# Optimization experiments

Measured on AMD Instinct MI355X. Metric: run time of the kernel, lower is better.

## Reference

```python
import jax, jax.numpy as jnp
import numpy as np

EPS = 1e-6
NUM_HEADS = 16

def _ln(x):
    # LayerNorm32, no affine, eps=1e-6, computed in fp32
    x32 = x.astype(jnp.float32)
    mu = jnp.mean(x32, axis=-1, keepdims=True)
    var = jnp.var(x32, axis=-1, keepdims=True)
    return ((x32 - mu) * jax.lax.rsqrt(var + EPS)).astype(x.dtype)

def _mha(q, k, v):
    # q,k,v: [B, L, H, D]
    d = q.shape[-1]
    scale = 1.0 / jnp.sqrt(jnp.asarray(d, q.dtype))
    s = jnp.einsum('bqhd,bkhd->bhqk', q, k) * scale
    p = jax.nn.softmax(s, axis=-1)
    o = jnp.einsum('bhqk,bkhd->bqhd', p, v)
    return o.reshape(o.shape[0], o.shape[1], -1)

def setup_inputs() -> dict:
    key = jax.random.key(0)
    ks = jax.random.split(key, 10)
    B, L, C, Lc, Cc = 4, 2048, 1024, 1024, 1024
    Dff = 4 * C
    s = 0.02
    return {
        'x': jax.random.normal(ks[0], (B, L, C), jnp.float32),
        'context': jax.random.normal(ks[1], (B, Lc, Cc), jnp.float32),
        'w_qkv': jax.random.normal(ks[2], (C, 3 * C), jnp.float32) * s,
        'b_qkv': jnp.zeros((3 * C,), jnp.float32),
        'w_os': jax.random.normal(ks[3], (C, C), jnp.float32) * s,
        'b_os': jnp.zeros((C,), jnp.float32),
        'w_qc': jax.random.normal(ks[4], (C, C), jnp.float32) * s,
        'b_qc': jnp.zeros((C,), jnp.float32),
        'w_kvc': jax.random.normal(ks[5], (Cc, 2 * C), jnp.float32) * s,
        'b_kvc': jnp.zeros((2 * C,), jnp.float32),
        'w_oc': jax.random.normal(ks[6], (C, C), jnp.float32) * s,
        'b_oc': jnp.zeros((C,), jnp.float32),
        'w_fc1': jax.random.normal(ks[7], (C, Dff), jnp.float32) * s,
        'b_fc1': jnp.zeros((Dff,), jnp.float32),
        'w_fc2': jax.random.normal(ks[8], (Dff, C), jnp.float32) * s,
        'b_fc2': jnp.zeros((C,), jnp.float32),
    }

def reference(x, context, w_qkv, b_qkv, w_os, b_os, w_qc, b_qc, w_kvc, b_kvc,
              w_oc, b_oc, w_fc1, b_fc1, w_fc2, b_fc2):
    B, L, C = x.shape
    H = NUM_HEADS
    D = C // H
    # --- self attention (pre-norm, full) ---
    h = _ln(x)
    qkv = (h @ w_qkv + b_qkv).reshape(B, L, 3, H, D)
    q, k, v = qkv[:, :, 0], qkv[:, :, 1], qkv[:, :, 2]
    h = _mha(q, k, v) @ w_os + b_os
    x = x + h
    # --- cross attention ---
    h = _ln(x)
    q = (h @ w_qc + b_qc).reshape(B, L, H, D)
    Lc = context.shape[1]
    kv = (context @ w_kvc + b_kvc).reshape(B, Lc, 2, H, D)
    k, v = kv[:, :, 0], kv[:, :, 1]
    h = _mha(q, k, v) @ w_oc + b_oc
    x = x + h
    # --- sparse FFN (GELU tanh) ---
    h = _ln(x)
    h = jax.nn.gelu(h @ w_fc1 + b_fc1, approximate=True) @ w_fc2 + b_fc2
    return x + h
```

## Files before the change

kernel.cpp:

```cpp
#include <hip/hip_runtime.h>

typedef unsigned short ushort_t;
typedef __attribute__((ext_vector_type(8))) short short8;
typedef __attribute__((ext_vector_type(4))) float f32x4;
typedef __attribute__((ext_vector_type(4))) unsigned short ushort4v;

__device__ inline ushort_t f2bf(float f) {
    union { float f; unsigned u; } v; v.f = f;
    return (ushort_t)((v.u + 0x7FFFu + ((v.u >> 16) & 1u)) >> 16);
}
__device__ inline float bf2f(ushort_t u) {
    union { unsigned u; float f; } v; v.u = ((unsigned)u) << 16;
    return v.f;
}

__device__ inline float fast_exp2(float x) {
#if __has_builtin(__builtin_amdgcn_exp2f)
    return __builtin_amdgcn_exp2f(x);
#else
    float r; asm("v_exp_f32 %0, %1" : "=v"(r) : "v"(x)); return r;
#endif
}

__device__ inline void gld16(const ushort_t* g, ushort_t* l) {
    __builtin_amdgcn_global_load_lds(
        (const __attribute__((address_space(1))) unsigned int*)g,
        (__attribute__((address_space(3))) unsigned int*)l, 16, 0, 0);
}

__device__ inline int xcd_swz(int id, int nwg) {
    int q = nwg >> 3;
    return (id & 7) * q + (id >> 3);
}

struct WPrep {
    const float* src[7];
    ushort_t*    dst[7];
    int K[7], N[7];
    int tilesBefore[8];
};

__global__ void w_prep_all(WPrep P) {
    __shared__ float t[64][65];
    const int bid = blockIdx.x;
    int e = 0;
#pragma unroll
    for (int i = 0; i < 7; i++) if (bid >= P.tilesBefore[i + 1]) e = i + 1;
    const int lt = bid - P.tilesBefore[e];
    const int K = P.K[e], N = P.N[e];
    const int ntx = N >> 6;
    const int n0 = (lt % ntx) * 64, k0 = (lt / ntx) * 64;
    const float* w = P.src[e];
    ushort_t* out = P.dst[e];
    const int tid = threadIdx.x;
#pragma unroll
    for (int i = 0; i < 16; i++) {
        int idx = tid + i * 256;
        int r = idx >> 6, c = idx & 63;
        t[r][c] = w[(size_t)(k0 + r) * N + n0 + c];
    }
    __syncthreads();
#pragma unroll
    for (int i = 0; i < 16; i++) {
        int idx = tid + i * 256;
        int nr = idx >> 6, kc = idx & 63;
        out[(size_t)(n0 + nr) * K + k0 + kc] = f2bf(t[kc][nr]);
    }
}

__global__ void v_transpose(const ushort_t* __restrict__ V, int vStride, int rowsPerBatch,
                            ushort_t* __restrict__ Vt, int Lk) {
    __shared__ __align__(16) ushort_t t[64][72];
    const int bh = blockIdx.y, k0 = blockIdx.x * 64;
    const int b = bh >> 4, h = bh & 15;
    const int tid = threadIdx.x;
    const ushort_t* src = V + (size_t)(b * rowsPerBatch + k0) * vStride + h * 64;
#pragma unroll
    for (int i = 0; i < 2; i++) {
        int ch = tid + i * 256;
        int r = ch >> 3, c = (ch & 7) * 8;
        *(short8*)(&t[r][c]) = *(const short8*)(src + (size_t)r * vStride + c);
    }
    __syncthreads();
#pragma unroll
    for (int i = 0; i < 2; i++) {
        int ch = tid + i * 256;
        int d = ch >> 3, c = (ch & 7) * 8;
        short8 o;
#pragma unroll
        for (int j = 0; j < 8; j++) o[j] = (short)t[c + j][d];
        *(short8*)(Vt + ((size_t)bh * 64 + d) * Lk + k0 + c) = o;
    }
}

__global__ void f32_to_bf16_vec(const float* __restrict__ in, ushort_t* __restrict__ out, int n4) {
    int i = blockIdx.x * blockDim.x + threadIdx.x;
    if (i < n4) {
        float4 v = ((const float4*)in)[i];
        ushort4v o;
        o[0] = f2bf(v.x); o[1] = f2bf(v.y); o[2] = f2bf(v.z); o[3] = f2bf(v.w);
        ((ushort4v*)out)[i] = o;
    }
}

__global__ void ln_rows(const float* __restrict__ in, ushort_t* __restrict__ out) {
    __shared__ float s1[4], s2[4];
    const int row = blockIdx.x;
    const int tid = threadIdx.x;
    const float4 v = ((const float4*)(in + (size_t)row * 1024))[tid];
    float s  = v.x + v.y + v.z + v.w;
    float ss = v.x * v.x + v.y * v.y + v.z * v.z + v.w * v.w;
#pragma unroll
    for (int d = 32; d >= 1; d >>= 1) {
        s  += __shfl_down(s, d, 64);
        ss += __shfl_down(ss, d, 64);
    }
    if ((tid & 63) == 0) { s1[tid >> 6] = s; s2[tid >> 6] = ss; }
    __syncthreads();
    float sum = s1[0] + s1[1] + s1[2] + s1[3];
    float sqs = s2[0] + s2[1] + s2[2] + s2[3];
    float mu  = sum * (1.0f / 1024.0f);
    float var = sqs * (1.0f / 1024.0f) - mu * mu;
    float rs  = rsqrtf(var + 1e-6f);
    ushort4v o;
    o[0] = f2bf((v.x - mu) * rs);
    o[1] = f2bf((v.y - mu) * rs);
    o[2] = f2bf((v.z - mu) * rs);
    o[3] = f2bf((v.w - mu) * rs);
    ((ushort4v*)(out + (size_t)row * 1024))[tid] = o;
}

#define EPI_BF16 0
#define EPI_GELU 1
#define EPI_RES  2

template <int EPI>
__global__ void gemm_bt(const ushort_t* __restrict__ A, const ushort_t* __restrict__ Bt,
                        const float* __restrict__ bias, const float* __restrict__ res,
                        void* __restrict__ outp, int M, int N, int K) {
    __shared__ __align__(16) ushort_t As[128 * 64];
    __shared__ __align__(16) ushort_t Bs[128 * 64];
    const int tid = threadIdx.x;
    const int lane = tid & 63, wave = tid >> 6;
    const int nwg = gridDim.x * gridDim.y;
    const int sid = xcd_swz(blockIdx.y * gridDim.x + blockIdx.x, nwg);
    const int m0 = (sid / gridDim.x) * 128, n0 = (sid % gridDim.x) * 128;
    const int wr = (wave >> 1) * 64, wc = (wave & 1) * 64;
    const int lr = lane & 15, lg = lane >> 4;

    f32x4 acc[4][4];
#pragma unroll
    for (int i = 0; i < 4; i++)
#pragma unroll
        for (int j = 0; j < 4; j++) acc[i][j] = f32x4{0.f, 0.f, 0.f, 0.f};

    for (int k0 = 0; k0 < K; k0 += 64) {
#pragma unroll
        for (int i = 0; i < 4; i++) {
            int ch = tid + i * 256;
            int r = ch >> 3;
            int kcs = (((ch & 7) ^ (r & 7))) * 8;
            gld16(A  + (size_t)(m0 + r) * K + k0 + kcs, As + ch * 8);
            gld16(Bt + (size_t)(n0 + r) * K + k0 + kcs, Bs + ch * 8);
        }
        __syncthreads();
#pragma unroll
        for (int ks = 0; ks < 2; ks++) {
            short8 af[4], bfr[4];
#pragma unroll
            for (int m = 0; m < 4; m++) {
                int r = wr + m * 16 + lr;
                int kc = ks * 4 + lg;
                af[m] = *(const short8*)(As + r * 64 + ((kc ^ (r & 7)) << 3));
            }
#pragma unroll
            for (int n = 0; n < 4; n++) {
                int r = wc + n * 16 + lr;
                int kc = ks * 4 + lg;
                bfr[n] = *(const short8*)(Bs + r * 64 + ((kc ^ (r & 7)) << 3));
            }
#pragma unroll
            for (int m = 0; m < 4; m++)
#pragma unroll
                for (int n = 0; n < 4; n++)
                    acc[m][n] = __builtin_amdgcn_mfma_f32_16x16x32_bf16(af[m], bfr[n], acc[m][n], 0, 0, 0);
        }
        __syncthreads();
    }

#pragma unroll
    for (int m = 0; m < 4; m++) {
        int rowb = m0 + wr + m * 16 + lg * 4;
#pragma unroll
        for (int n = 0; n < 4; n++) {
            int col = n0 + wc + n * 16 + lr;
            float bcol = bias[col];
            f32x4 v = acc[m][n];
#pragma unroll
            for (int q = 0; q < 4; q++) {
                float x = v[q] + bcol;
                if (EPI == EPI_GELU) {
                    float u = 0.7978845608028654f * (x + 0.044715f * x * x * x);
                    float a = fabsf(u);
                    float tt = fast_exp2(-2.885390081777927f * a);
                    float th = copysignf((1.0f - tt) / (1.0f + tt), u);
                    x = 0.5f * x * (1.0f + th);
                }
                size_t off = (size_t)(rowb + q) * N + col;
                if (EPI == EPI_RES) ((float*)outp)[off] = x + res[off];
                else                ((ushort_t*)outp)[off] = f2bf(x);
            }
        }
    }
}

__global__ __launch_bounds__(512, 2)
void attn_fwd(const ushort_t* __restrict__ Q, int qStride,
              const ushort_t* __restrict__ Kp, int kvStride, int kvBatchRows,
              const ushort_t* __restrict__ Vt, int Lk,
              ushort_t* __restrict__ O) {
    __shared__ __align__(16) ushort_t Ks[2][64 * 64];
    __shared__ __align__(16) ushort_t Vts[2][64 * 64];
    __shared__ __align__(16) ushort_t Ps[8][16 * 64];
    const int tid = threadIdx.x, lane = tid & 63, wave = tid >> 6;
    const int lr = lane & 15, lg = lane >> 4;
    const int sid = xcd_swz(blockIdx.x, gridDim.x);
    const int qb = sid & 7, h = (sid >> 3) & 15, b = sid >> 7;
    const int qRow0 = b * 2048 + qb * 256;
    const int kvRow0 = b * kvBatchRows;
    const int hc = h * 64;
    const ushort_t* vt_base = Vt + (size_t)(b * 16 + h) * 64 * Lk;

    short8 qf[2][2];
#pragma unroll
    for (int qh = 0; qh < 2; qh++) {
        const ushort_t* qrow = Q + (size_t)(qRow0 + wave * 32 + qh * 16 + lr) * qStride + hc;
        short8 r0 = *(const short8*)(qrow + lg * 8);
        short8 r1 = *(const short8*)(qrow + 32 + lg * 8);
        const float s = 0.125f * 1.4426950408889634f;
#pragma unroll
        for (int j = 0; j < 8; j++) {
            qf[qh][0][j] = (short)f2bf(bf2f((ushort_t)r0[j]) * s);
            qf[qh][1][j] = (short)f2bf(bf2f((ushort_t)r1[j]) * s);
        }
    }

    f32x4 oacc[2][4];
#pragma unroll
    for (int qh = 0; qh < 2; qh++)
#pragma unroll
        for (int d = 0; d < 4; d++) oacc[qh][d] = f32x4{0.f, 0.f, 0.f, 0.f};
    float mrun[2] = {-1e30f, -1e30f}, lrun[2] = {0.f, 0.f};

    const int nt = Lk >> 6;

    auto stage = [&](int buf, int kt) {
        int r = tid >> 3;
        int kcs = (((tid & 7) ^ (r & 7))) * 8;
        gld16(Kp + (size_t)(kvRow0 + kt + r) * kvStride + hc + kcs, Ks[buf] + tid * 8);
        gld16(vt_base + (size_t)r * Lk + kt + kcs, Vts[buf] + tid * 8);
    };

    stage(0, 0);
    __syncthreads();
    int cur = 0;

    for (int t = 0; t < nt; ++t) {
        if (t + 1 < nt) stage(cur ^ 1, (t + 1) * 64);

        const ushort_t* Kc = Ks[cur];
        const ushort_t* Vc = Vts[cur];

        f32x4 sacc[2][4];
        __builtin_amdgcn_s_setprio(1);
#pragma unroll
        for (int n = 0; n < 4; n++) {
            int r = n * 16 + lr;
            short8 k0 = *(const short8*)(Kc + r * 64 + ((lg ^ (r & 7)) << 3));
            short8 k1 = *(const short8*)(Kc + r * 64 + (((4 + lg) ^ (r & 7)) << 3));
#pragma unroll
            for (int qh = 0; qh < 2; qh++) {
                f32x4 s = f32x4{0.f, 0.f, 0.f, 0.f};
                s = __builtin_amdgcn_mfma_f32_16x16x32_bf16(k0, qf[qh][0], s, 0, 0, 0);
                s = __builtin_amdgcn_mfma_f32_16x16x32_bf16(k1, qf[qh][1], s, 0, 0, 0);
                sacc[qh][n] = s;
            }
        }
        __builtin_amdgcn_s_setprio(0);

        short8 pf[2][2];
        ushort_t* Pw = &Ps[wave][0];
#pragma unroll
        for (int qh = 0; qh < 2; qh++) {
            float mx = sacc[qh][0][0];
#pragma unroll
            for (int n = 0; n < 4; n++)
#pragma unroll
                for (int r = 0; r < 4; r++) if (n | r) mx = fmaxf(mx, sacc[qh][n][r]);
            mx = fmaxf(mx, __shfl_xor(mx, 16, 64));
            mx = fmaxf(mx, __shfl_xor(mx, 32, 64));

            if (!__all(mx <= mrun[qh] + 11.5416f)) {
                float mnew = fmaxf(mrun[qh], mx);
                float al = fast_exp2(mrun[qh] - mnew);
                float a0 = __shfl(al, lg * 4 + 0, 64);
                float a1 = __shfl(al, lg * 4 + 1, 64);
                float a2 = __shfl(al, lg * 4 + 2, 64);
                float a3 = __shfl(al, lg * 4 + 3, 64);
#pragma unroll
                for (int dn = 0; dn < 4; dn++) {
                    oacc[qh][dn][0] *= a0; oacc[qh][dn][1] *= a1;
                    oacc[qh][dn][2] *= a2; oacc[qh][dn][3] *= a3;
                }
                lrun[qh] *= al;
                mrun[qh] = mnew;
            }

            float rsum = 0.f;
#pragma unroll
            for (int n = 0; n < 4; n++)
#pragma unroll
                for (int r = 0; r < 4; r++) {
                    float p = fast_exp2(sacc[qh][n][r] - mrun[qh]);
                    sacc[qh][n][r] = p;
                    rsum += p;
                }
            rsum += __shfl_xor(rsum, 16, 64);
            rsum += __shfl_xor(rsum, 32, 64);
            lrun[qh] += rsum;

#pragma unroll
            for (int n = 0; n < 4; n++) {
                unsigned w0, w1;
                asm("v_cvt_pk_bf16_f32 %0, %1, %2" : "=v"(w0) : "v"(sacc[qh][n][0]), "v"(sacc[qh][n][1]));
                asm("v_cvt_pk_bf16_f32 %0, %1, %2" : "=v"(w1) : "v"(sacc[qh][n][2]), "v"(sacc[qh][n][3]));
                int kc = n * 2 + (lg >> 1);
                uint2 u; u.x = w0; u.y = w1;
                *(uint2*)((char*)Pw + lr * 128 + ((kc ^ (lr & 7)) << 4) + (lg & 1) * 8) = u;
            }
            pf[qh][0] = *(const short8*)(Pw + lr * 64 + ((lg ^ (lr & 7)) << 3));
            pf[qh][1] = *(const short8*)(Pw + lr * 64 + (((4 + lg) ^ (lr & 7)) << 3));
        }

        __builtin_amdgcn_s_setprio(1);
#pragma unroll
        for (int dn = 0; dn < 4; dn++) {
            int r = dn * 16 + lr;
            short8 v0 = *(const short8*)(Vc + r * 64 + ((lg ^ (r & 7)) << 3));
            short8 v1 = *(const short8*)(Vc + r * 64 + (((4 + lg) ^ (r & 7)) << 3));
#pragma unroll
            for (int qh = 0; qh < 2; qh++) {
                oacc[qh][dn] = __builtin_amdgcn_mfma_f32_16x16x32_bf16(pf[qh][0], v0, oacc[qh][dn], 0, 0, 0);
                oacc[qh][dn] = __builtin_amdgcn_mfma_f32_16x16x32_bf16(pf[qh][1], v1, oacc[qh][dn], 0, 0, 0);
            }
        }
        __builtin_amdgcn_s_setprio(0);
        __syncthreads();
        cur ^= 1;
    }

#pragma unroll
    for (int qh = 0; qh < 2; qh++) {
        float linv[4];
#pragma unroll
        for (int r = 0; r < 4; r++) linv[r] = 1.0f / __shfl(lrun[qh], lg * 4 + r, 64);
#pragma unroll
        for (int dn = 0; dn < 4; dn++)
#pragma unroll
            for (int q = 0; q < 4; q++) {
                float o = oacc[qh][dn][q] * linv[q];
                int row = qRow0 + wave * 32 + qh * 16 + lg * 4 + q;
                int col = hc + dn * 16 + lr;
                O[(size_t)row * 1024 + col] = f2bf(o);
            }
    }
}

extern "C" void kernel_launch(void* const* d_in, const int* in_sizes, int n_in,
                              void* d_out, int out_size, void* d_ws, size_t ws_size,
                              hipStream_t stream) {
    const float* x     = (const float*)d_in[0];
    const float* ctx   = (const float*)d_in[1];
    const float* w_qkv = (const float*)d_in[2];
    const float* b_qkv = (const float*)d_in[3];
    const float* w_os  = (const float*)d_in[4];
    const float* b_os  = (const float*)d_in[5];
    const float* w_qc  = (const float*)d_in[6];
    const float* b_qc  = (const float*)d_in[7];
    const float* w_kvc = (const float*)d_in[8];
    const float* b_kvc = (const float*)d_in[9];
    const float* w_oc  = (const float*)d_in[10];
    const float* b_oc  = (const float*)d_in[11];
    const float* w_fc1 = (const float*)d_in[12];
    const float* b_fc1 = (const float*)d_in[13];
    const float* w_fc2 = (const float*)d_in[14];
    const float* b_fc2 = (const float*)d_in[15];
    float* out = (float*)d_out;

    char* ws = (char*)d_ws;
    ushort_t* wqkvT = (ushort_t*)(ws + 0);
    ushort_t* wosT  = (ushort_t*)(ws + 6291456);
    ushort_t* wqcT  = (ushort_t*)(ws + 8388608);
    ushort_t* wkvcT = (ushort_t*)(ws + 10485760);
    ushort_t* wocT  = (ushort_t*)(ws + 14680064);
    ushort_t* wfc1T = (ushort_t*)(ws + 16777216);
    ushort_t* wfc2T = (ushort_t*)(ws + 25165824);
    ushort_t* qkv_bf  = (ushort_t*)(ws + 33554432);
    ushort_t* q_bf    = (ushort_t*)(ws + 33554432);
    ushort_t* kv_bf   = (ushort_t*)(ws + 50331648);
    ushort_t* vt_c    = (ushort_t*)(ws + 67108864);
    ushort_t* ffn_bf  = (ushort_t*)(ws + 33554432);
    ushort_t* ctx_bf  = (ushort_t*)(ws + 83886080);
    ushort_t* attn_bf = (ushort_t*)(ws + 92274688);
    ushort_t* h_bf    = (ushort_t*)(ws + 109051904);
    ushort_t* vt_s    = (ushort_t*)(ws + 109051904);

    const dim3 tb(256);
    const dim3 tb512(512);

    WPrep P;
    P.src[0] = w_qkv; P.dst[0] = wqkvT; P.K[0] = 1024; P.N[0] = 3072;
    P.src[1] = w_os;  P.dst[1] = wosT;  P.K[1] = 1024; P.N[1] = 1024;
    P.src[2] = w_qc;  P.dst[2] = wqcT;  P.K[2] = 1024; P.N[2] = 1024;
    P.src[3] = w_kvc; P.dst[3] = wkvcT; P.K[3] = 1024; P.N[3] = 2048;
    P.src[4] = w_oc;  P.dst[4] = wocT;  P.K[4] = 1024; P.N[4] = 1024;
    P.src[5] = w_fc1; P.dst[5] = wfc1T; P.K[5] = 1024; P.N[5] = 4096;
    P.src[6] = w_fc2; P.dst[6] = wfc2T; P.K[6] = 4096; P.N[6] = 1024;
    P.tilesBefore[0] = 0;
    for (int i = 0; i < 7; i++)
        P.tilesBefore[i + 1] = P.tilesBefore[i] + (P.N[i] / 64) * (P.K[i] / 64);
    w_prep_all<<<dim3(P.tilesBefore[7]), tb, 0, stream>>>(P);
    f32_to_bf16_vec<<<4096, tb, 0, stream>>>(ctx, ctx_bf, 1048576);

    ln_rows<<<8192, tb, 0, stream>>>(x, h_bf);
    gemm_bt<EPI_BF16><<<dim3(24, 64), tb, 0, stream>>>(h_bf, wqkvT, b_qkv, nullptr, qkv_bf, 8192, 3072, 1024);
    v_transpose<<<dim3(32, 64), tb, 0, stream>>>(qkv_bf + 2048, 3072, 2048, vt_s, 2048);
    attn_fwd<<<dim3(512), tb512, 0, stream>>>(qkv_bf, 3072, qkv_bf + 1024, 3072, 2048,
                                              vt_s, 2048, attn_bf);
    gemm_bt<EPI_RES><<<dim3(8, 64), tb, 0, stream>>>(attn_bf, wosT, b_os, x, out, 8192, 1024, 1024);

    ln_rows<<<8192, tb, 0, stream>>>(out, h_bf);
    gemm_bt<EPI_BF16><<<dim3(8, 64), tb, 0, stream>>>(h_bf, wqcT, b_qc, nullptr, q_bf, 8192, 1024, 1024);
    gemm_bt<EPI_BF16><<<dim3(16, 32), tb, 0, stream>>>(ctx_bf, wkvcT, b_kvc, nullptr, kv_bf, 4096, 2048, 1024);
    v_transpose<<<dim3(16, 64), tb, 0, stream>>>(kv_bf + 1024, 2048, 1024, vt_c, 1024);
    attn_fwd<<<dim3(512), tb512, 0, stream>>>(q_bf, 1024, kv_bf, 2048, 1024,
                                              vt_c, 1024, attn_bf);
    gemm_bt<EPI_RES><<<dim3(8, 64), tb, 0, stream>>>(attn_bf, wocT, b_oc, out, out, 8192, 1024, 1024);

    ln_rows<<<8192, tb, 0, stream>>>(out, h_bf);
    gemm_bt<EPI_GELU><<<dim3(32, 64), tb, 0, stream>>>(h_bf, wfc1T, b_fc1, nullptr, ffn_bf, 8192, 4096, 1024);
    gemm_bt<EPI_RES><<<dim3(8, 64), tb, 0, stream>>>(ffn_bf, wfc2T, b_fc2, out, out, 8192, 1024, 4096);
}
```

Measured before the change: 550.3 us.

## Fold running max into MFMA accumulator and compute row sums via MFMA

The score accumulator is initialised with the negative running max, so the QK^T MFMA yields already-shifted logits and the per-element subtraction disappears from the common path. Row sums of P are computed by extra MFMAs against a ones vector instead of a VALU reduction plus cross-lane shuffles. The max reduction is split into two chains for more instruction-level parallelism. In exchange each tile issues four more MFMAs, and the row sum now accumulates the bf16-rounded probabilities, which shifts numerics slightly.

```diff
diff --git a/kernel.cpp b/kernel.cpp
--- a/kernel.cpp
+++ b/kernel.cpp
@@ -245,12 +245,19 @@
         }
     }
 
+    short8 vone;
+#pragma unroll
+    for (int j = 0; j < 8; j++) vone[j] = (lr == 0) ? (short)0x3F80 : (short)0;
+
     f32x4 oacc[2][4];
-#pragma unroll
-    for (int qh = 0; qh < 2; qh++)
+    f32x4 lsum[2];
+#pragma unroll
+    for (int qh = 0; qh < 2; qh++) {
 #pragma unroll
         for (int d = 0; d < 4; d++) oacc[qh][d] = f32x4{0.f, 0.f, 0.f, 0.f};
-    float mrun[2] = {-1e30f, -1e30f}, lrun[2] = {0.f, 0.f};
+        lsum[qh] = f32x4{0.f, 0.f, 0.f, 0.f};
+    }
+    float mrun[2] = {0.f, 0.f};
 
     const int nt = Lk >> 6;
 
@@ -272,6 +279,12 @@
         const ushort_t* Vc = Vts[cur];
 
         f32x4 sacc[2][4];
+#pragma unroll
+        for (int qh = 0; qh < 2; qh++) {
+            float m = -mrun[qh];
+#pragma unroll
+            for (int n = 0; n < 4; n++) sacc[qh][n] = f32x4{m, m, m, m};
+        }
         __builtin_amdgcn_s_setprio(1);
 #pragma unroll
         for (int n = 0; n < 4; n++) {
@@ -280,10 +293,8 @@
             short8 k1 = *(const short8*)(Kc + r * 64 + (((4 + lg) ^ (r & 7)) << 3));
 #pragma unroll
             for (int qh = 0; qh < 2; qh++) {
-                f32x4 s = f32x4{0.f, 0.f, 0.f, 0.f};
-                s = __builtin_amdgcn_mfma_f32_16x16x32_bf16(k0, qf[qh][0], s, 0, 0, 0);
-                s = __builtin_amdgcn_mfma_f32_16x16x32_bf16(k1, qf[qh][1], s, 0, 0, 0);
-                sacc[qh][n] = s;
+                sacc[qh][n] = __builtin_amdgcn_mfma_f32_16x16x32_bf16(k0, qf[qh][0], sacc[qh][n], 0, 0, 0);
+                sacc[qh][n] = __builtin_amdgcn_mfma_f32_16x16x32_bf16(k1, qf[qh][1], sacc[qh][n], 0, 0, 0);
             }
         }
         __builtin_amdgcn_s_setprio(0);
@@ -292,17 +303,20 @@
         ushort_t* Pw = &Ps[wave][0];
 #pragma unroll
         for (int qh = 0; qh < 2; qh++) {
-            float mx = sacc[qh][0][0];
-#pragma unroll
-            for (int n = 0; n < 4; n++)
-#pragma unroll
-                for (int r = 0; r < 4; r++) if (n | r) mx = fmaxf(mx, sacc[qh][n][r]);
+            float m01 = fmaxf(sacc[qh][0][0], sacc[qh][0][1]);
+            float m23 = fmaxf(sacc[qh][0][2], sacc[qh][0][3]);
+#pragma unroll
+            for (int n = 1; n < 4; n++) {
+                m01 = fmaxf(m01, fmaxf(sacc[qh][n][0], sacc[qh][n][1]));
+                m23 = fmaxf(m23, fmaxf(sacc[qh][n][2], sacc[qh][n][3]));
+            }
+            float mx = fmaxf(m01, m23);
             mx = fmaxf(mx, __shfl_xor(mx, 16, 64));
             mx = fmaxf(mx, __shfl_xor(mx, 32, 64));
 
-            if (!__all(mx <= mrun[qh] + 11.5416f)) {
-                float mnew = fmaxf(mrun[qh], mx);
-                float al = fast_exp2(mrun[qh] - mnew);
+            if (!__all(mx <= 11.5416f)) {
+                float d = fmaxf(mx, 0.0f);
+                float al = fast_exp2(-d);
                 float a0 = __shfl(al, lg * 4 + 0, 64);
                 float a1 = __shfl(al, lg * 4 + 1, 64);
                 float a2 = __shfl(al, lg * 4 + 2, 64);
@@ -312,22 +326,19 @@
                     oacc[qh][dn][0] *= a0; oacc[qh][dn][1] *= a1;
                     oacc[qh][dn][2] *= a2; oacc[qh][dn][3] *= a3;
                 }
-                lrun[qh] *= al;
-                mrun[qh] = mnew;
-            }
-
-            float rsum = 0.f;
+                lsum[qh][0] *= a0; lsum[qh][1] *= a1;
+                lsum[qh][2] *= a2; lsum[qh][3] *= a3;
+                mrun[qh] += d;
+#pragma unroll
+                for (int n = 0; n < 4; n++)
+#pragma unroll
+                    for (int r = 0; r < 4; r++) sacc[qh][n][r] -= d;
+            }
+
 #pragma unroll
             for (int n = 0; n < 4; n++)
 #pragma unroll
-                for (int r = 0; r < 4; r++) {
-                    float p = fast_exp2(sacc[qh][n][r] - mrun[qh]);
-                    sacc[qh][n][r] = p;
-                    rsum += p;
-                }
-            rsum += __shfl_xor(rsum, 16, 64);
-            rsum += __shfl_xor(rsum, 32, 64);
-            lrun[qh] += rsum;
+                for (int r = 0; r < 4; r++) sacc[qh][n][r] = fast_exp2(sacc[qh][n][r]);
 
 #pragma unroll
             for (int n = 0; n < 4; n++) {
@@ -354,6 +365,11 @@
                 oacc[qh][dn] = __builtin_amdgcn_mfma_f32_16x16x32_bf16(pf[qh][1], v1, oacc[qh][dn], 0, 0, 0);
             }
         }
+#pragma unroll
+        for (int qh = 0; qh < 2; qh++) {
+            lsum[qh] = __builtin_amdgcn_mfma_f32_16x16x32_bf16(pf[qh][0], vone, lsum[qh], 0, 0, 0);
+            lsum[qh] = __builtin_amdgcn_mfma_f32_16x16x32_bf16(pf[qh][1], vone, lsum[qh], 0, 0, 0);
+        }
         __builtin_amdgcn_s_setprio(0);
         __syncthreads();
         cur ^= 1;
@@ -363,7 +379,7 @@
     for (int qh = 0; qh < 2; qh++) {
         float linv[4];
 #pragma unroll
-        for (int r = 0; r < 4; r++) linv[r] = 1.0f / __shfl(lrun[qh], lg * 4 + r, 64);
+        for (int q = 0; q < 4; q++) linv[q] = 1.0f / __shfl(lsum[qh][q], lg * 16, 64);
 #pragma unroll
         for (int dn = 0; dn < 4; dn++)
 #pragma unroll
```

Result: slower. 573.4 us (+4.2%).
